# Kernel tuning notes

Hardware: AMD Instinct MI355X
Metric: run time of the kernel (lower is better)

The kernel has to match this reference:

```python
import jax, jax.numpy as jnp
import numpy as np

N, E, D, H = 50000, 600000, 128, 128
SLOPE = 0.01  # default negative_slope of F.leaky_relu / nn.LeakyReLU


def leaky(x):
    return jnp.where(x >= 0, x, SLOPE * x)


def gcn_conv(x, src, dst, W, b, n):
    """PyG GCNConv: x' = D^{-1/2}(A+I)D^{-1/2} (x W) + b, symmetric norm with self-loops."""
    h = x @ W  # [n, out]
    ones = jnp.ones(src.shape[0], h.dtype)
    deg = jax.ops.segment_sum(ones, dst, num_segments=n) + 1.0  # +1 for self-loop
    dinv = jax.lax.rsqrt(deg)  # deg >= 1 always
    norm = dinv[src] * dinv[dst]  # per-edge coefficient
    msg = h[src] * norm[:, None]  # gather + scale: [E, out]
    agg = jax.ops.segment_sum(msg, dst, num_segments=n)  # scatter-add
    agg = agg + h * (dinv * dinv)[:, None]  # self-loop term
    return agg + b


def setup_inputs() -> dict:
    key = jax.random.key(0)
    ks = jax.random.split(key, 16)
    kaiming = lambda k, fi, fo: jax.random.normal(k, (fi, fo), jnp.float32) * np.sqrt(2.0 / fi)
    return {
        "x": jax.random.normal(ks[0], (N, D), jnp.float32),
        "edge_index": jax.random.randint(ks[1], (2, E), 0, N, jnp.int64 if jax.config.jax_enable_x64 else jnp.int32),
        "gen_data": jax.random.normal(ks[2], (N, H), jnp.float32),
        "Wc1": kaiming(ks[3], D, H), "bc1": jnp.zeros((H,), jnp.float32),
        "Wc2": kaiming(ks[4], H, H), "bc2": jnp.zeros((H,), jnp.float32),
        "Wm1": kaiming(ks[5], H, H), "bm1": jnp.zeros((H,), jnp.float32),
        "Wm2": kaiming(ks[6], H, H), "bm2": jnp.zeros((H,), jnp.float32),
        "Wp1": kaiming(ks[7], H, H), "bp1": jnp.zeros((H,), jnp.float32),
        "Wp2": kaiming(ks[8], H, H), "bp2": jnp.zeros((H,), jnp.float32),
    }


def reference(x, edge_index, gen_data, Wc1, bc1, Wc2, bc2, Wm1, bm1, Wm2, bm2, Wp1, bp1, Wp2, bp2):
    src, dst = edge_index[0], edge_index[1]
    lambd = 0.5
    # GraphEncoder4Link
    h = leaky(gcn_conv(x, src, dst, Wc1, bc1, N))
    h = leaky(gcn_conv(h, src, dst, Wc2, bc2, N) + h)
    h = leaky((leaky(h @ Wm1 + bm1) @ Wm2 + bm2) + h)
    # lambd interpolation with gen_data
    out = lambd * h + (1.0 - lambd) * gen_data
    # proj MLP
    out = leaky(leaky(out @ Wp1 + bp1) @ Wp2 + bp2)
    return out
```

## Files before the change

kernel.cpp:

```cpp
#include <hip/hip_runtime.h>
#include <cstdint>
#include <cstddef>

#define HH 128
#define SLOPE 0.01f

typedef __attribute__((ext_vector_type(8))) __bf16 bf16x8;
typedef __attribute__((ext_vector_type(8))) unsigned short ushort8v;
typedef __attribute__((ext_vector_type(4))) float f32x4;

__device__ __forceinline__ float lrelu(float x) { return x >= 0.f ? x : SLOPE * x; }
__device__ __forceinline__ unsigned short f2b(float f) {
  union { float f; unsigned u; } v; v.f = f;
  unsigned r = v.u + 0x7fffu + ((v.u >> 16) & 1u);
  return (unsigned short)(r >> 16);
}
__device__ __forceinline__ float b2f(unsigned short u) {
  union { unsigned u; float f; } v; v.u = ((unsigned)u) << 16; return v.f;
}

__device__ __forceinline__ int lofs(int r, int k) {
  return (r << 7) + ((((k >> 3) ^ r) & 15) << 3) + (k & 7);
}

#define WAVE_SYNC() asm volatile("s_waitcnt lgkmcnt(0)" ::: "memory")

__device__ __forceinline__ void gll16(const void* g, void* l) {
  __builtin_amdgcn_global_load_lds((const __attribute__((address_space(1))) void*)g,
                                   (__attribute__((address_space(3))) void*)l, 16, 0, 0);
}


__global__ __launch_bounds__(256) void count_kernel(const int* __restrict__ dst,
                                                    int* __restrict__ cnt,
                                                    int* __restrict__ rank, int nE) {
  int e = blockIdx.x * 256 + threadIdx.x;
  if (e < nE) rank[e] = atomicAdd(&cnt[dst[e]], 1);
}

__global__ __launch_bounds__(1024) void scan1_kernel(int* __restrict__ cnt,
                                                     int* __restrict__ rowptr,
                                                     int* __restrict__ bsum,
                                                     float* __restrict__ dinv, int n) {
  __shared__ int wsum[16];
  const int tid = threadIdx.x;
  const int lane = tid & 63, wid = tid >> 6;
  int i = blockIdx.x * 1024 + tid;
  int v = (i < n) ? cnt[i] : 0;
  int vp = (v + 7) & ~7;
  int x = vp;
#pragma unroll
  for (int off = 1; off < 64; off <<= 1) {
    int y = __shfl_up(x, off, 64);
    if (lane >= off) x += y;
  }
  if (lane == 63) wsum[wid] = x;
  __syncthreads();
  if (tid == 0) {
    int s = 0;
#pragma unroll
    for (int w = 0; w < 16; ++w) { int t = wsum[w]; wsum[w] = s; s += t; }
    bsum[blockIdx.x] = s;
  }
  __syncthreads();
  if (i < n) {
    rowptr[i] = wsum[wid] + x - vp;
    dinv[i] = rsqrtf((float)v + 1.0f);
  }
}

__global__ __launch_bounds__(64) void scan2_kernel(int* __restrict__ bsum, int nb,
                                                   int* __restrict__ rowptr, int n) {
  int lane = threadIdx.x;
  int v = (lane < nb) ? bsum[lane] : 0;
  int x = v;
#pragma unroll
  for (int off = 1; off < 64; off <<= 1) {
    int y = __shfl_up(x, off, 64);
    if (lane >= off) x += y;
  }
  int tot = __shfl(x, nb - 1);
  if (lane < nb) bsum[lane] = x - v;
  if (lane == 0) rowptr[n] = tot;
}

__global__ __launch_bounds__(1024) void scan3_kernel(int* __restrict__ rowptr,
                                                     const int* __restrict__ bsum, int n) {
  int i = blockIdx.x * 1024 + threadIdx.x;
  if (i < n) rowptr[i] += bsum[blockIdx.x];
}

__global__ __launch_bounds__(256) void fill_kernel(const int* __restrict__ src,
                                                   const int* __restrict__ dst,
                                                   const int* __restrict__ rowptr,
                                                   const int* __restrict__ rank,
                                                   const float* __restrict__ dinv,
                                                   int2* __restrict__ csr, int nE) {
  int e = blockIdx.x * 256 + threadIdx.x;
  if (e >= nE) return;
  int d = dst[e], s = src[e];
  int pos = rowptr[d] + rank[e];
  int2 ent;
  ent.x = s;
  ent.y = __float_as_int(dinv[s] * dinv[d]);
  csr[pos] = ent;
}

__global__ __launch_bounds__(256) void pack_kernel(const float* W0, const float* W1,
                                                   const float* W2, const float* W3,
                                                   const float* W4, const float* W5,
                                                   unsigned short* __restrict__ out) {
  const float* Ws[6] = {W0, W1, W2, W3, W4, W5};
  const float* W = Ws[blockIdx.y];
  int f = blockIdx.x * 256 + threadIdx.x;
  int j = f & 7, L = (f >> 3) & 63, c = (f >> 9) & 7, t = f >> 12;
  int k = t * 32 + (L >> 4) * 8 + j;
  int n = c * 16 + (L & 15);
  out[(size_t)blockIdx.y * 16384 + f] = f2b(W[k * HH + n]);
}


__device__ __forceinline__ void mfma_ldsW(const bf16x8 af[4],
                                          const unsigned short* __restrict__ Wl,
                                          int lane, f32x4 acc[8]) {
#pragma unroll
  for (int c = 0; c < 8; ++c) acc[c] = (f32x4){0.f, 0.f, 0.f, 0.f};
#pragma unroll
  for (int t = 0; t < 4; ++t) {
    bf16x8 wf[8];
#pragma unroll
    for (int c = 0; c < 8; ++c) wf[c] = *(const bf16x8*)&Wl[(t * 8 + c) * 512 + lane * 8];
#pragma unroll
    for (int c = 0; c < 8; ++c)
      acc[c] = __builtin_amdgcn_mfma_f32_16x16x32_bf16(af[t], wf[c], acc[c], 0, 0, 0);
  }
}

__device__ __forceinline__ void lds_afrags16(const unsigned short* __restrict__ Tl,
                                             int m, int quad, bf16x8 af[4]) {
#pragma unroll
  for (int t = 0; t < 4; ++t)
    af[t] = *(const bf16x8*)&Tl[lofs(m, t * 32 + quad * 8)];
}


__global__ __launch_bounds__(256, 1) void gemm_conv(const float* __restrict__ A,
                                                    const unsigned short* __restrict__ Wp,
                                                    unsigned short* __restrict__ out, int nrows) {
  __shared__ __align__(16) unsigned short Wl[16384];
  const int tid = threadIdx.x;
  const int lane = tid & 63, wave = tid >> 6;
  const int row0 = blockIdx.x * 64 + wave * 16;
  const int m = lane & 15, quad = lane >> 4;

#pragma unroll
  for (int i = 0; i < 8; ++i)
    gll16((const uint4*)Wp + i * 256 + tid, (uint4*)Wl + i * 256 + wave * 64);

  const int gr = row0 + m;
  const bool rok = gr < nrows;
  const float* Arow = A + (size_t)gr * HH;
  bf16x8 af[4];
#pragma unroll
  for (int t = 0; t < 4; ++t) {
    const int k = t * 32 + quad * 8;
    float4 lo = make_float4(0.f, 0.f, 0.f, 0.f), hi = lo;
    if (rok) {
      lo = *(const float4*)(Arow + k);
      hi = *(const float4*)(Arow + k + 4);
    }
    union { ushort8v u; bf16x8 b; } cv;
    cv.u[0] = f2b(lo.x); cv.u[1] = f2b(lo.y); cv.u[2] = f2b(lo.z); cv.u[3] = f2b(lo.w);
    cv.u[4] = f2b(hi.x); cv.u[5] = f2b(hi.y); cv.u[6] = f2b(hi.z); cv.u[7] = f2b(hi.w);
    af[t] = cv.b;
  }

  __syncthreads();

  f32x4 acc[8];
  mfma_ldsW(af, Wl, lane, acc);

#pragma unroll
  for (int c = 0; c < 8; ++c) {
    int col = c * 16 + m;
#pragma unroll
    for (int g = 0; g < 4; ++g) {
      int row = row0 + quad * 4 + g;
      if (row < nrows) out[(size_t)row * HH + col] = f2b(acc[c][g]);
    }
  }
}


template <int RES, int OUTBF>
__global__ __launch_bounds__(256) void agg_kernel(const unsigned short* __restrict__ h,
                                                  const int* __restrict__ rowptr,
                                                  const int2* __restrict__ csr,
                                                  const float* __restrict__ dinv,
                                                  const float* __restrict__ bias,
                                                  const float* __restrict__ res,
                                                  void* __restrict__ outv, int n) {
  int node = blockIdx.x * 4 + (threadIdx.x >> 6);
  if (node >= n) return;
  const int lane = threadIdx.x & 63;
  const int p = lane >> 5;
  const int c4 = (lane & 31) << 2;
  int j = rowptr[node];
  const int end = rowptr[node + 1];

  const float di = dinv[node];
  const ushort4 hs = *(const ushort4*)(h + (size_t)node * HH + c4);
  const float4 b = *(const float4*)(bias + c4);
  float4 rr = make_float4(0.f, 0.f, 0.f, 0.f);
  if (RES) rr = *(const float4*)(res + (size_t)node * HH + c4);

  float a0 = 0.f, a1 = 0.f, a2 = 0.f, a3 = 0.f;
  for (; j < end; j += 8) {
    int2 e[4];
    ushort4 r[4];
#pragma unroll
    for (int q = 0; q < 4; ++q) e[q] = csr[j + 2 * q + p];
#pragma unroll
    for (int q = 0; q < 4; ++q) r[q] = *(const ushort4*)(h + (size_t)e[q].x * HH + c4);
#pragma unroll
    for (int q = 0; q < 4; ++q) {
      float nv = __int_as_float(e[q].y);
      a0 = fmaf(b2f(r[q].x), nv, a0); a1 = fmaf(b2f(r[q].y), nv, a1);
      a2 = fmaf(b2f(r[q].z), nv, a2); a3 = fmaf(b2f(r[q].w), nv, a3);
    }
  }

  a0 += __shfl_xor(a0, 32);
  a1 += __shfl_xor(a1, 32);
  a2 += __shfl_xor(a2, 32);
  a3 += __shfl_xor(a3, 32);

  if (p == 0) {
    const float d2 = di * di;
    float o0 = a0 + b2f(hs.x) * d2 + b.x + rr.x;
    float o1 = a1 + b2f(hs.y) * d2 + b.y + rr.y;
    float o2 = a2 + b2f(hs.z) * d2 + b.z + rr.z;
    float o3 = a3 + b2f(hs.w) * d2 + b.w + rr.w;
    o0 = lrelu(o0); o1 = lrelu(o1); o2 = lrelu(o2); o3 = lrelu(o3);
    if (OUTBF) {
      ushort4 o;
      o.x = f2b(o0); o.y = f2b(o1); o.z = f2b(o2); o.w = f2b(o3);
      *(ushort4*)((unsigned short*)outv + (size_t)node * HH + c4) = o;
    } else {
      *(float4*)((float*)outv + (size_t)node * HH + c4) = make_float4(o0, o1, o2, o3);
    }
  }
}


__global__ __launch_bounds__(256, 1) void fusedMLP(const unsigned short* __restrict__ f2bf,
                                                   const unsigned short* __restrict__ Wm1p,
                                                   const unsigned short* __restrict__ Wm2p,
                                                   const unsigned short* __restrict__ Wp1p,
                                                   const unsigned short* __restrict__ Wp2p,
                                                   const float* __restrict__ bm1,
                                                   const float* __restrict__ bm2,
                                                   const float* __restrict__ bp1,
                                                   const float* __restrict__ bp2,
                                                   const float* __restrict__ gen,
                                                   float* __restrict__ out, int n) {
  __shared__ __align__(16) unsigned short Wl[16384];
  __shared__ __align__(16) unsigned short Ta[4][16 * HH];
  __shared__ __align__(16) unsigned short Tb[4][16 * HH];
  __shared__ __align__(16) float Bi[4][4 * HH];
  const int tid = threadIdx.x;
  const int lane = tid & 63, wave = tid >> 6;
  const int row0 = blockIdx.x * 64 + wave * 16;
  const int m = lane & 15, quad = lane >> 4;
  unsigned short* TA = Ta[wave];
  unsigned short* TB = Tb[wave];
  float* BI = Bi[wave];

#pragma unroll
  for (int i = 0; i < 8; ++i)
    gll16((const uint4*)Wm1p + i * 256 + tid, (uint4*)Wl + i * 256 + wave * 64);

#pragma unroll
  for (int i = 0; i < 4; ++i) {
    int idx = i * 64 + lane;
    int r = idx >> 4, k = (idx & 15) << 3;
    int gr = row0 + r;
    ushort8v v = {0, 0, 0, 0, 0, 0, 0, 0};
    if (gr < n) v = *(const ushort8v*)(f2bf + (size_t)gr * HH + k);
    *(ushort8v*)&TA[lofs(r, k)] = v;
  }

  ushort4 genb[8];
#pragma unroll
  for (int i = 0; i < 8; ++i) {
    int idx = i * 64 + lane;
    int r = idx >> 5, c4 = (idx & 31) << 2;
    int gr = row0 + r;
    float4 v = make_float4(0.f, 0.f, 0.f, 0.f);
    if (gr < n) v = *(const float4*)(gen + (size_t)gr * HH + c4);
    genb[i].x = f2b(v.x); genb[i].y = f2b(v.y); genb[i].z = f2b(v.z); genb[i].w = f2b(v.w);
  }

  {
    const float* b01 = (lane < 32) ? bm1 : bm2;
    const float* b23 = (lane < 32) ? bp1 : bp2;
    int col = (lane & 31) << 2;
    float4 v0 = *(const float4*)(b01 + col);
    float4 v1 = *(const float4*)(b23 + col);
    *(float4*)&BI[lane * 4] = v0;
    *(float4*)&BI[256 + lane * 4] = v1;
  }

  __syncthreads();

  bf16x8 af[4];
  f32x4 acc[8];
  float bv[8];

#pragma unroll
  for (int cc = 0; cc < 8; ++cc) bv[cc] = BI[cc * 16 + m];
  lds_afrags16(TA, m, quad, af);
  mfma_ldsW(af, Wl, lane, acc);
#pragma unroll
  for (int cc = 0; cc < 8; ++cc) {
    int col = cc * 16 + m;
#pragma unroll
    for (int g = 0; g < 4; ++g)
      TB[lofs(quad * 4 + g, col)] = f2b(lrelu(acc[cc][g] + bv[cc]));
  }
  __syncthreads();

#pragma unroll
  for (int i = 0; i < 8; ++i)
    gll16((const uint4*)Wm2p + i * 256 + tid, (uint4*)Wl + i * 256 + wave * 64);
#pragma unroll
  for (int cc = 0; cc < 8; ++cc) bv[cc] = BI[128 + cc * 16 + m];
  lds_afrags16(TB, m, quad, af);
  WAVE_SYNC();
#pragma unroll
  for (int i = 0; i < 8; ++i) {
    int idx = i * 64 + lane;
    int r = idx >> 5, c4 = (idx & 31) << 2;
    *(ushort4*)&TB[lofs(r, c4)] = genb[i];
  }
  __syncthreads();

  mfma_ldsW(af, Wl, lane, acc);
#pragma unroll
  for (int cc = 0; cc < 8; ++cc) {
    int col = cc * 16 + m;
#pragma unroll
    for (int g = 0; g < 4; ++g) {
      int lr = quad * 4 + g;
      float f2v = b2f(TA[lofs(lr, col)]);
      float v = lrelu(acc[cc][g] + bv[cc] + f2v);
      float gv = b2f(TB[lofs(lr, col)]);
      TA[lofs(lr, col)] = f2b(0.5f * (v + gv));
    }
  }
  __syncthreads();

#pragma unroll
  for (int i = 0; i < 8; ++i)
    gll16((const uint4*)Wp1p + i * 256 + tid, (uint4*)Wl + i * 256 + wave * 64);
#pragma unroll
  for (int cc = 0; cc < 8; ++cc) bv[cc] = BI[256 + cc * 16 + m];
  lds_afrags16(TA, m, quad, af);
  __syncthreads();

  mfma_ldsW(af, Wl, lane, acc);
#pragma unroll
  for (int cc = 0; cc < 8; ++cc) {
    int col = cc * 16 + m;
#pragma unroll
    for (int g = 0; g < 4; ++g)
      TB[lofs(quad * 4 + g, col)] = f2b(lrelu(acc[cc][g] + bv[cc]));
  }
  __syncthreads();

#pragma unroll
  for (int i = 0; i < 8; ++i)
    gll16((const uint4*)Wp2p + i * 256 + tid, (uint4*)Wl + i * 256 + wave * 64);
#pragma unroll
  for (int cc = 0; cc < 8; ++cc) bv[cc] = BI[384 + cc * 16 + m];
  lds_afrags16(TB, m, quad, af);
  __syncthreads();

  mfma_ldsW(af, Wl, lane, acc);
#pragma unroll
  for (int cc = 0; cc < 8; ++cc) {
    int col = cc * 16 + m;
#pragma unroll
    for (int g = 0; g < 4; ++g) {
      int row = row0 + quad * 4 + g;
      if (row < n) out[(size_t)row * HH + col] = lrelu(acc[cc][g] + bv[cc]);
    }
  }
}


extern "C" void kernel_launch(void* const* d_in, const int* in_sizes, int n_in,
                              void* d_out, int out_size, void* d_ws, size_t ws_size,
                              hipStream_t stream) {
  const float* x   = (const float*)d_in[0];
  const int* ei    = (const int*)d_in[1];
  const float* gen = (const float*)d_in[2];
  const float* Wc1 = (const float*)d_in[3];
  const float* bc1 = (const float*)d_in[4];
  const float* Wc2 = (const float*)d_in[5];
  const float* bc2 = (const float*)d_in[6];
  const float* Wm1 = (const float*)d_in[7];
  const float* bm1 = (const float*)d_in[8];
  const float* Wm2 = (const float*)d_in[9];
  const float* bm2 = (const float*)d_in[10];
  const float* Wp1 = (const float*)d_in[11];
  const float* bp1 = (const float*)d_in[12];
  const float* Wp2 = (const float*)d_in[13];
  const float* bp2 = (const float*)d_in[14];

  const int N = in_sizes[0] / HH;
  const int E = in_sizes[1] / 2;
  const int* src = ei;
  const int* dst = ei + E;

  const size_t Epad = (size_t)E + 8 * (size_t)N;

  char* ws = (char*)d_ws;
  size_t off = 0;
  auto alloc = [&](size_t bytes) { void* p = ws + off; off += (bytes + 255) & ~(size_t)255; return p; };
  float* dinv            = (float*)alloc((size_t)N * 4);
  int*   rowptr          = (int*)  alloc((size_t)(N + 1) * 4);
  int*   cnt             = (int*)  alloc((size_t)N * 4);
  int*   bsum            = (int*)  alloc((size_t)64 * 4);
  int*   rank            = (int*)  alloc((size_t)E * 4);
  int2*  csr             = (int2*) alloc(Epad * 8);
  unsigned short* h_bf   = (unsigned short*)alloc((size_t)N * HH * 2);
  unsigned short* t2_bf  = (unsigned short*)alloc((size_t)N * HH * 2);
  unsigned short* f2_bf  = (unsigned short*)alloc((size_t)N * HH * 2);
  float* f1_f32          = (float*)alloc((size_t)N * HH * 4);
  unsigned short* packed = (unsigned short*)alloc((size_t)6 * 16384 * 2);
  float* fOut = (float*)d_out;

  const int cblocks = (N + 63) / 64;
  const int eblocks = (E + 255) / 256;
  const int ablocks = (N + 3) / 4;
  const int sblocks = (N + 1023) / 1024;

  pack_kernel<<<dim3(64, 6), 256, 0, stream>>>(Wc1, Wc2, Wm1, Wm2, Wp1, Wp2, packed);

  hipMemsetAsync(cnt, 0, (size_t)N * 4, stream);
  hipMemsetAsync(csr, 0, Epad * 8, stream);
  count_kernel<<<eblocks, 256, 0, stream>>>(dst, cnt, rank, E);
  scan1_kernel<<<sblocks, 1024, 0, stream>>>(cnt, rowptr, bsum, dinv, N);
  scan2_kernel<<<1, 64, 0, stream>>>(bsum, sblocks, rowptr, N);
  scan3_kernel<<<sblocks, 1024, 0, stream>>>(rowptr, bsum, N);
  fill_kernel<<<eblocks, 256, 0, stream>>>(src, dst, rowptr, rank, dinv, csr, E);

  gemm_conv<<<cblocks, 256, 0, stream>>>(x, packed + 0 * 16384, h_bf, N);
  agg_kernel<0, 0><<<ablocks, 256, 0, stream>>>(h_bf, rowptr, csr, dinv, bc1, nullptr, f1_f32, N);
  gemm_conv<<<cblocks, 256, 0, stream>>>(f1_f32, packed + 1 * 16384, t2_bf, N);
  agg_kernel<1, 1><<<ablocks, 256, 0, stream>>>(t2_bf, rowptr, csr, dinv, bc2, f1_f32, f2_bf, N);
  fusedMLP<<<cblocks, 256, 0, stream>>>(f2_bf,
                                        packed + 2 * 16384, packed + 3 * 16384,
                                        packed + 4 * 16384, packed + 5 * 16384,
                                        bm1, bm2, bp1, bp2, gen, fOut, N);
}
```

Measured before the change: 278.0 us.

## Double-buffer MLP weights in LDS and prefetch next layer during compute

The fused MLP kernel now keeps two weight buffers in LDS, so each layer's weights are loaded while the previous layer's MFMAs run. This cuts the number of block-wide barriers between the four GEMMs. The separate activation buffers merge into one per-wave tile, with the residual kept in registers. Biases now load straight into registers instead of staging through LDS. LDS use stays about the same, but register pressure rises from the cached residual and bias arrays.

```diff
diff --git a/kernel.cpp b/kernel.cpp
--- a/kernel.cpp
+++ b/kernel.cpp
@@ -264,21 +264,19 @@
                                                    const float* __restrict__ bp2,
                                                    const float* __restrict__ gen,
                                                    float* __restrict__ out, int n) {
-  __shared__ __align__(16) unsigned short Wl[16384];
-  __shared__ __align__(16) unsigned short Ta[4][16 * HH];
-  __shared__ __align__(16) unsigned short Tb[4][16 * HH];
-  __shared__ __align__(16) float Bi[4][4 * HH];
+  __shared__ __align__(16) unsigned short Wl[2][16384];
+  __shared__ __align__(16) unsigned short Tl[4][16 * HH];
   const int tid = threadIdx.x;
   const int lane = tid & 63, wave = tid >> 6;
   const int row0 = blockIdx.x * 64 + wave * 16;
   const int m = lane & 15, quad = lane >> 4;
-  unsigned short* TA = Ta[wave];
-  unsigned short* TB = Tb[wave];
-  float* BI = Bi[wave];
-
-#pragma unroll
-  for (int i = 0; i < 8; ++i)
-    gll16((const uint4*)Wm1p + i * 256 + tid, (uint4*)Wl + i * 256 + wave * 64);
+  unsigned short* T = Tl[wave];
+
+#pragma unroll
+  for (int i = 0; i < 8; ++i) {
+    gll16((const uint4*)Wm1p + i * 256 + tid, (uint4*)Wl[0] + i * 256 + wave * 64);
+    gll16((const uint4*)Wm2p + i * 256 + tid, (uint4*)Wl[1] + i * 256 + wave * 64);
+  }
 
 #pragma unroll
   for (int i = 0; i < 4; ++i) {
@@ -287,7 +285,7 @@
     int gr = row0 + r;
     ushort8v v = {0, 0, 0, 0, 0, 0, 0, 0};
     if (gr < n) v = *(const ushort8v*)(f2bf + (size_t)gr * HH + k);
-    *(ushort8v*)&TA[lofs(r, k)] = v;
+    *(ushort8v*)&T[lofs(r, k)] = v;
   }
 
   ushort4 genb[8];
@@ -301,99 +299,97 @@
     genb[i].x = f2b(v.x); genb[i].y = f2b(v.y); genb[i].z = f2b(v.z); genb[i].w = f2b(v.w);
   }
 
-  {
-    const float* b01 = (lane < 32) ? bm1 : bm2;
-    const float* b23 = (lane < 32) ? bp1 : bp2;
-    int col = (lane & 31) << 2;
-    float4 v0 = *(const float4*)(b01 + col);
-    float4 v1 = *(const float4*)(b23 + col);
-    *(float4*)&BI[lane * 4] = v0;
-    *(float4*)&BI[256 + lane * 4] = v1;
+  float bvAll[4][8];
+#pragma unroll
+  for (int cc = 0; cc < 8; ++cc) {
+    int col = cc * 16 + m;
+    bvAll[0][cc] = bm1[col];
+    bvAll[1][cc] = bm2[col];
+    bvAll[2][cc] = bp1[col];
+    bvAll[3][cc] = bp2[col];
   }
 
   __syncthreads();
 
   bf16x8 af[4];
   f32x4 acc[8];
-  float bv[8];
-
-#pragma unroll
-  for (int cc = 0; cc < 8; ++cc) bv[cc] = BI[cc * 16 + m];
-  lds_afrags16(TA, m, quad, af);
-  mfma_ldsW(af, Wl, lane, acc);
+
+  lds_afrags16(T, m, quad, af);
+  unsigned f2res[8][2];
+#pragma unroll
+  for (int cc = 0; cc < 8; ++cc) {
+    int col = cc * 16 + m;
+#pragma unroll
+    for (int gp = 0; gp < 2; ++gp) {
+      int lr = quad * 4 + gp * 2;
+      f2res[cc][gp] = (unsigned)T[lofs(lr, col)] | ((unsigned)T[lofs(lr + 1, col)] << 16);
+    }
+  }
+  mfma_ldsW(af, Wl[0], lane, acc);
+  WAVE_SYNC();
 #pragma unroll
   for (int cc = 0; cc < 8; ++cc) {
     int col = cc * 16 + m;
 #pragma unroll
     for (int g = 0; g < 4; ++g)
-      TB[lofs(quad * 4 + g, col)] = f2b(lrelu(acc[cc][g] + bv[cc]));
+      T[lofs(quad * 4 + g, col)] = f2b(lrelu(acc[cc][g] + bvAll[0][cc]));
   }
   __syncthreads();
 
 #pragma unroll
   for (int i = 0; i < 8; ++i)
-    gll16((const uint4*)Wm2p + i * 256 + tid, (uint4*)Wl + i * 256 + wave * 64);
-#pragma unroll
-  for (int cc = 0; cc < 8; ++cc) bv[cc] = BI[128 + cc * 16 + m];
-  lds_afrags16(TB, m, quad, af);
+    gll16((const uint4*)Wp1p + i * 256 + tid, (uint4*)Wl[0] + i * 256 + wave * 64);
+
+  lds_afrags16(T, m, quad, af);
   WAVE_SYNC();
 #pragma unroll
   for (int i = 0; i < 8; ++i) {
     int idx = i * 64 + lane;
     int r = idx >> 5, c4 = (idx & 31) << 2;
-    *(ushort4*)&TB[lofs(r, c4)] = genb[i];
-  }
-  __syncthreads();
-
-  mfma_ldsW(af, Wl, lane, acc);
+    *(ushort4*)&T[lofs(r, c4)] = genb[i];
+  }
+  mfma_ldsW(af, Wl[1], lane, acc);
+  WAVE_SYNC();
 #pragma unroll
   for (int cc = 0; cc < 8; ++cc) {
     int col = cc * 16 + m;
 #pragma unroll
     for (int g = 0; g < 4; ++g) {
       int lr = quad * 4 + g;
-      float f2v = b2f(TA[lofs(lr, col)]);
-      float v = lrelu(acc[cc][g] + bv[cc] + f2v);
-      float gv = b2f(TB[lofs(lr, col)]);
-      TA[lofs(lr, col)] = f2b(0.5f * (v + gv));
+      unsigned fr = f2res[cc][g >> 1];
+      float f2v = b2f((unsigned short)((g & 1) ? (fr >> 16) : (fr & 0xffffu)));
+      float v = lrelu(acc[cc][g] + bvAll[1][cc] + f2v);
+      float gv = b2f(T[lofs(lr, col)]);
+      T[lofs(lr, col)] = f2b(0.5f * (v + gv));
     }
   }
   __syncthreads();
 
 #pragma unroll
   for (int i = 0; i < 8; ++i)
-    gll16((const uint4*)Wp1p + i * 256 + tid, (uint4*)Wl + i * 256 + wave * 64);
-#pragma unroll
-  for (int cc = 0; cc < 8; ++cc) bv[cc] = BI[256 + cc * 16 + m];
-  lds_afrags16(TA, m, quad, af);
-  __syncthreads();
-
-  mfma_ldsW(af, Wl, lane, acc);
+    gll16((const uint4*)Wp2p + i * 256 + tid, (uint4*)Wl[1] + i * 256 + wave * 64);
+
+  lds_afrags16(T, m, quad, af);
+  mfma_ldsW(af, Wl[0], lane, acc);
+  WAVE_SYNC();
 #pragma unroll
   for (int cc = 0; cc < 8; ++cc) {
     int col = cc * 16 + m;
 #pragma unroll
     for (int g = 0; g < 4; ++g)
-      TB[lofs(quad * 4 + g, col)] = f2b(lrelu(acc[cc][g] + bv[cc]));
-  }
-  __syncthreads();
-
-#pragma unroll
-  for (int i = 0; i < 8; ++i)
-    gll16((const uint4*)Wp2p + i * 256 + tid, (uint4*)Wl + i * 256 + wave * 64);
-#pragma unroll
-  for (int cc = 0; cc < 8; ++cc) bv[cc] = BI[384 + cc * 16 + m];
-  lds_afrags16(TB, m, quad, af);
-  __syncthreads();
-
-  mfma_ldsW(af, Wl, lane, acc);
+      T[lofs(quad * 4 + g, col)] = f2b(lrelu(acc[cc][g] + bvAll[2][cc]));
+  }
+  __syncthreads();
+
+  lds_afrags16(T, m, quad, af);
+  mfma_ldsW(af, Wl[1], lane, acc);
 #pragma unroll
   for (int cc = 0; cc < 8; ++cc) {
     int col = cc * 16 + m;
 #pragma unroll
     for (int g = 0; g < 4; ++g) {
       int row = row0 + quad * 4 + g;
-      if (row < n) out[(size_t)row * HH + col] = lrelu(acc[cc][g] + bv[cc]);
+      if (row < n) out[(size_t)row * HH + col] = lrelu(acc[cc][g] + bvAll[3][cc]);
     }
   }
 }
```

New measurement: 280.8 us. No clear change (+1.0%).
